# Kernel tuning notes

Measured on AMD Instinct MI355X. Metric: run time of the kernel, lower is better.

## Reference

```python
import jax, jax.numpy as jnp
import numpy as np

NUM_SEQS = 64
NUM_HEADS = 32
NUM_KV_HEADS = 8
HEAD_SIZE = 128
BLOCK_SIZE = 16
X = 8  # key cache vector width (16 bytes / fp16 elem size in vLLM)
NUM_BLOCKS = 4096
MAX_BLOCKS_PER_SEQ = 64
MAX_CTX = MAX_BLOCKS_PER_SEQ * BLOCK_SIZE  # 1024
SCALE = 0.08838834764831845  # 1/sqrt(HEAD_SIZE)
Q_PER_KV = NUM_HEADS // NUM_KV_HEADS


def setup_inputs() -> dict:
    key = jax.random.key(0)
    k0, k1, k2, k3, k4 = jax.random.split(key, 5)
    query = jax.random.normal(k0, (NUM_SEQS, NUM_HEADS, HEAD_SIZE), dtype=jnp.float32)
    key_cache = jax.random.normal(
        k1, (NUM_BLOCKS, NUM_KV_HEADS, HEAD_SIZE // X, BLOCK_SIZE, X), dtype=jnp.float32)
    value_cache = jax.random.normal(
        k2, (NUM_BLOCKS, NUM_KV_HEADS, HEAD_SIZE, BLOCK_SIZE), dtype=jnp.float32)
    block_tables = jax.random.randint(
        k3, (NUM_SEQS, MAX_BLOCKS_PER_SEQ), 0, NUM_BLOCKS, dtype=jnp.int32)
    context_lens = jax.random.randint(k4, (NUM_SEQS,), 1, MAX_CTX + 1, dtype=jnp.int32)
    return {"query": query, "key_cache": key_cache, "value_cache": value_cache,
            "block_tables": block_tables, "context_lens": context_lens}


def _paged_attention(query, key_cache, value_cache, block_tables, context_lens):
    nb = key_cache.shape[0]
    # key cache [nb, kvH, hs//x, bs, x] -> [nb, kvH, bs, hs]
    k_tok = jnp.transpose(key_cache, (0, 1, 3, 2, 4)).reshape(nb, NUM_KV_HEADS, BLOCK_SIZE, HEAD_SIZE)
    # value cache [nb, kvH, hs, bs] -> [nb, kvH, bs, hs]
    v_tok = jnp.transpose(value_cache, (0, 1, 3, 2))
    # gather per-sequence paged KV via block tables: [S, MB, kvH, bs, hs] -> [S, MAX_CTX, kvH, hs]
    keys = k_tok[block_tables].transpose(0, 1, 3, 2, 4).reshape(NUM_SEQS, MAX_CTX, NUM_KV_HEADS, HEAD_SIZE)
    values = v_tok[block_tables].transpose(0, 1, 3, 2, 4).reshape(NUM_SEQS, MAX_CTX, NUM_KV_HEADS, HEAD_SIZE)
    # GQA: group query heads over kv heads. q4: [S, kvH, qpkv, hs]
    q4 = query.reshape(NUM_SEQS, NUM_KV_HEADS, Q_PER_KV, HEAD_SIZE)
    # scores: [S, kvH, qpkv, MAX_CTX]
    scores = jnp.einsum('sgqd,skgd->sgqk', q4, keys) * SCALE
    valid = jnp.arange(MAX_CTX, dtype=jnp.int32)[None, :] < context_lens[:, None]  # [S, K]
    scores = jnp.where(valid[:, None, None, :], scores, jnp.float32(-1e30))
    probs = jax.nn.softmax(scores, axis=-1)
    out = jnp.einsum('sgqk,skgd->sgqd', probs, values)
    return out.reshape(NUM_SEQS, NUM_HEADS, HEAD_SIZE)


def reference(query, key_cache, value_cache, block_tables, context_lens):
    return _paged_attention(query, key_cache, value_cache, block_tables, context_lens)
```

## Files before the change

kernel.cpp:

```cpp
#include <hip/hip_runtime.h>

#define NSEQ   64
#define NHEAD  32
#define KVH    8
#define HS     128
#define BS     16
#define MBPS   64
#define MAXCTX 1024
#define QPKV   4
#define SCALE_F 0.08838834764831845f

__launch_bounds__(256)
__global__ void pa_kernel(const float* __restrict__ q,
                          const float* __restrict__ kc,
                          const float* __restrict__ vc,
                          const int*   __restrict__ bt,
                          const int*   __restrict__ cl,
                          float*       __restrict__ out)
{
    const int seq = blockIdx.x >> 3;
    const int kvh = blockIdx.x & 7;
    const int t   = threadIdx.x;
    const int ctx = cl[seq];
    const int nb  = (ctx + BS - 1) / BS;

    __shared__ __align__(16) float sc[QPKV][MAXCTX + 8];
    __shared__ float qs[QPKV][HS];
    __shared__ float l_inv[QPKV];

    for (int i = t; i < QPKV * HS; i += 256) {
        int g = i >> 7, d = i & 127;
        qs[g][d] = q[((size_t)seq * NHEAD + kvh * QPKV + g) * HS + d];
    }
    __syncthreads();

    const int tok   = t >> 4;
    const int dpart = t & 15;
    float qreg[QPKV][8];
#pragma unroll
    for (int g = 0; g < QPKV; ++g)
#pragma unroll
        for (int j = 0; j < 8; ++j)
            qreg[g][j] = qs[g][dpart * 8 + j];

    const int* btrow = bt + seq * MBPS;
    for (int b = 0; b < nb; ++b) {
        const int blk = btrow[b];
        const float* kptr = kc + ((size_t)blk * KVH + kvh) * (HS * BS)
                               + dpart * (BS * 8) + tok * 8;
        const float4 k0 = *(const float4*)kptr;
        const float4 k1 = *(const float4*)(kptr + 4);
        const float kk[8] = {k0.x,k0.y,k0.z,k0.w,k1.x,k1.y,k1.z,k1.w};
        float p[QPKV];
#pragma unroll
        for (int g = 0; g < QPKV; ++g) {
            float s = 0.f;
#pragma unroll
            for (int j = 0; j < 8; ++j) s += qreg[g][j] * kk[j];
            p[g] = s;
        }
#pragma unroll
        for (int off = 8; off >= 1; off >>= 1)
#pragma unroll
            for (int g = 0; g < QPKV; ++g)
                p[g] += __shfl_xor(p[g], off, 16);
        if (dpart < QPKV)
            sc[dpart][b * BS + tok] = p[dpart] * SCALE_F;
    }
    __syncthreads();

    {
        const int w    = t >> 6;
        const int lane = t & 63;
        float m = -1e30f;
        for (int i = lane; i < ctx; i += 64) m = fmaxf(m, sc[w][i]);
#pragma unroll
        for (int off = 32; off >= 1; off >>= 1) m = fmaxf(m, __shfl_xor(m, off));
        float ssum = 0.f;
        const int lim = nb * BS;
        for (int i = lane; i < lim; i += 64) {
            float v = (i < ctx) ? __expf(sc[w][i] - m) : 0.f;
            sc[w][i] = v;
            ssum += v;
        }
#pragma unroll
        for (int off = 32; off >= 1; off >>= 1) ssum += __shfl_xor(ssum, off);
        if (lane == 0) l_inv[w] = 1.f / ssum;
    }
    __syncthreads();

    const int d  = t >> 1;
    const int th = t & 1;
    float acc[QPKV] = {0.f, 0.f, 0.f, 0.f};
    for (int b = 0; b < nb; ++b) {
        const int blk = btrow[b];
        const float* vptr = vc + ((size_t)blk * KVH + kvh) * (HS * BS)
                               + d * BS + th * 8;
        const float4 v0 = *(const float4*)vptr;
        const float4 v1 = *(const float4*)(vptr + 4);
        const float vv[8] = {v0.x,v0.y,v0.z,v0.w,v1.x,v1.y,v1.z,v1.w};
        const int base = b * BS + th * 8;
#pragma unroll
        for (int g = 0; g < QPKV; ++g) {
            const float4 p0 = *(const float4*)&sc[g][base];
            const float4 p1 = *(const float4*)&sc[g][base + 4];
            acc[g] += p0.x*vv[0] + p0.y*vv[1] + p0.z*vv[2] + p0.w*vv[3]
                    + p1.x*vv[4] + p1.y*vv[5] + p1.z*vv[6] + p1.w*vv[7];
        }
    }
#pragma unroll
    for (int g = 0; g < QPKV; ++g)
        acc[g] += __shfl_xor(acc[g], 1);
    if (th == 0) {
#pragma unroll
        for (int g = 0; g < QPKV; ++g)
            out[((size_t)seq * NHEAD + kvh * QPKV + g) * HS + d] = acc[g] * l_inv[g];
    }
}

extern "C" void kernel_launch(void* const* d_in, const int* in_sizes, int n_in,
                              void* d_out, int out_size, void* d_ws, size_t ws_size,
                              hipStream_t stream) {
    const float* query       = (const float*)d_in[0];
    const float* key_cache   = (const float*)d_in[1];
    const float* value_cache = (const float*)d_in[2];
    const int*   block_tables= (const int*)d_in[3];
    const int*   context_lens= (const int*)d_in[4];
    float* out = (float*)d_out;

    dim3 grid(NSEQ * KVH);
    dim3 block(256);
    pa_kernel<<<grid, block, 0, stream>>>(query, key_cache, value_cache,
                                          block_tables, context_lens, out);
}
```

Measured before the change: 479.7 us.

## Split context into chunks with partial softmax and a separate reduce kernel

Replaces the single per-(sequence, kv-head) kernel with a flash-decoding style split: each workgroup handles an 8-block context chunk, producing a partial output plus its local max and exp-sum in workspace. A second kernel rescales and combines the chunks into the final output. This raises the workgroup count to fill the GPU and reduce load imbalance from variable context lengths, at the cost of an extra launch and workspace traffic. The old kernel is kept as a fallback when workspace is too small.

```diff
diff --git a/kernel.cpp b/kernel.cpp
--- a/kernel.cpp
+++ b/kernel.cpp
@@ -9,6 +9,162 @@
 #define MAXCTX 1024
 #define QPKV   4
 #define SCALE_F 0.08838834764831845f
+
+#define CB     8
+#define CTOK   (CB * BS)
+#define NCHUNK (MBPS / CB)
+#define NPART  (NSEQ * KVH * QPKV * NCHUNK)
+#define WS_BYTES ((size_t)(NPART * HS + 2 * NPART) * 4)
+
+__launch_bounds__(256)
+__global__ void pa_partial(const float* __restrict__ q,
+                           const float* __restrict__ kc,
+                           const float* __restrict__ vc,
+                           const int*   __restrict__ bt,
+                           const int*   __restrict__ cl,
+                           float*       __restrict__ opart,
+                           float*       __restrict__ mpart,
+                           float*       __restrict__ lpart)
+{
+    const int wg  = blockIdx.x;
+    const int kvh = wg & 7;
+    const int c   = (wg >> 3) & (NCHUNK - 1);
+    const int seq = wg >> 6;
+
+    const int ctx = cl[seq];
+    const int nb  = (ctx + BS - 1) >> 4;
+    const int b0  = c * CB;
+    if (b0 >= nb) return;
+    const int nbc = min(nb - b0, CB);
+    const int t   = threadIdx.x;
+
+    __shared__ __align__(16) float sc[QPKV][CTOK + 8];
+    __shared__ float qs[QPKV][HS];
+
+    for (int i = t; i < QPKV * HS; i += 256) {
+        int g = i >> 7, d = i & 127;
+        qs[g][d] = q[((size_t)seq * NHEAD + kvh * QPKV + g) * HS + d];
+    }
+    __syncthreads();
+
+    const int tok   = t >> 4;
+    const int dpart = t & 15;
+    float qreg[QPKV][8];
+#pragma unroll
+    for (int g = 0; g < QPKV; ++g)
+#pragma unroll
+        for (int j = 0; j < 8; ++j)
+            qreg[g][j] = qs[g][dpart * 8 + j];
+
+    const int* btrow = bt + seq * MBPS + b0;
+    for (int b = 0; b < nbc; ++b) {
+        const int blk = btrow[b];
+        const float* kptr = kc + ((size_t)blk * KVH + kvh) * (HS * BS)
+                               + dpart * (BS * 8) + tok * 8;
+        const float4 k0 = *(const float4*)kptr;
+        const float4 k1 = *(const float4*)(kptr + 4);
+        const float kk[8] = {k0.x,k0.y,k0.z,k0.w,k1.x,k1.y,k1.z,k1.w};
+        float p[QPKV];
+#pragma unroll
+        for (int g = 0; g < QPKV; ++g) {
+            float s = 0.f;
+#pragma unroll
+            for (int j = 0; j < 8; ++j) s += qreg[g][j] * kk[j];
+            p[g] = s;
+        }
+#pragma unroll
+        for (int off = 8; off >= 1; off >>= 1)
+#pragma unroll
+            for (int g = 0; g < QPKV; ++g)
+                p[g] += __shfl_xor(p[g], off, 16);
+        if (dpart < QPKV)
+            sc[dpart][b * BS + tok] = p[dpart] * SCALE_F;
+    }
+    __syncthreads();
+
+    {
+        const int w     = t >> 6;
+        const int lane  = t & 63;
+        const int lim   = nbc * BS;
+        const int valid = min(ctx - c * CTOK, lim);
+        float m = -1e30f;
+        for (int i = lane; i < valid; i += 64) m = fmaxf(m, sc[w][i]);
+#pragma unroll
+        for (int off = 32; off >= 1; off >>= 1) m = fmaxf(m, __shfl_xor(m, off));
+        float ssum = 0.f;
+        for (int i = lane; i < lim; i += 64) {
+            float v = (i < valid) ? __expf(sc[w][i] - m) : 0.f;
+            sc[w][i] = v;
+            ssum += v;
+        }
+#pragma unroll
+        for (int off = 32; off >= 1; off >>= 1) ssum += __shfl_xor(ssum, off);
+        if (lane == 0) {
+            const int pidx = ((seq * KVH + kvh) * QPKV + w) * NCHUNK + c;
+            mpart[pidx] = m;
+            lpart[pidx] = ssum;
+        }
+    }
+    __syncthreads();
+
+    const int d  = t >> 1;
+    const int th = t & 1;
+    float acc[QPKV] = {0.f, 0.f, 0.f, 0.f};
+    for (int b = 0; b < nbc; ++b) {
+        const int blk = btrow[b];
+        const float* vptr = vc + ((size_t)blk * KVH + kvh) * (HS * BS)
+                               + d * BS + th * 8;
+        const float4 v0 = *(const float4*)vptr;
+        const float4 v1 = *(const float4*)(vptr + 4);
+        const float vv[8] = {v0.x,v0.y,v0.z,v0.w,v1.x,v1.y,v1.z,v1.w};
+        const int base = b * BS + th * 8;
+#pragma unroll
+        for (int g = 0; g < QPKV; ++g) {
+            const float4 p0 = *(const float4*)&sc[g][base];
+            const float4 p1 = *(const float4*)&sc[g][base + 4];
+            acc[g] += p0.x*vv[0] + p0.y*vv[1] + p0.z*vv[2] + p0.w*vv[3]
+                    + p1.x*vv[4] + p1.y*vv[5] + p1.z*vv[6] + p1.w*vv[7];
+        }
+    }
+#pragma unroll
+    for (int g = 0; g < QPKV; ++g)
+        acc[g] += __shfl_xor(acc[g], 1);
+    if (th == 0) {
+#pragma unroll
+        for (int g = 0; g < QPKV; ++g)
+            opart[((size_t)((seq * KVH + kvh) * QPKV + g) * NCHUNK + c) * HS + d] = acc[g];
+    }
+}
+
+__launch_bounds__(128)
+__global__ void pa_reduce(const float* __restrict__ opart,
+                          const float* __restrict__ mpart,
+                          const float* __restrict__ lpart,
+                          const int*   __restrict__ cl,
+                          float*       __restrict__ out)
+{
+    const int wg  = blockIdx.x;
+    const int seq = wg >> 3;
+    const int d   = threadIdx.x;
+    const int ctx = cl[seq];
+    const int nb  = (ctx + BS - 1) >> 4;
+    const int nch = min((nb + CB - 1) / CB, NCHUNK);
+    const int kvh = wg & 7;
+
+#pragma unroll
+    for (int g = 0; g < QPKV; ++g) {
+        const int base = (wg * QPKV + g) * NCHUNK;
+        float M = -1e30f;
+        for (int c2 = 0; c2 < nch; ++c2) M = fmaxf(M, mpart[base + c2]);
+        float L = 0.f, o = 0.f;
+        for (int c2 = 0; c2 < nch; ++c2) {
+            const float w = __expf(mpart[base + c2] - M);
+            L += lpart[base + c2] * w;
+            o += opart[(size_t)(base + c2) * HS + d] * w;
+        }
+        out[((size_t)seq * NHEAD + kvh * QPKV + g) * HS + d] = o / L;
+    }
+}
 
 __launch_bounds__(256)
 __global__ void pa_kernel(const float* __restrict__ q,
@@ -121,15 +277,24 @@
 extern "C" void kernel_launch(void* const* d_in, const int* in_sizes, int n_in,
                               void* d_out, int out_size, void* d_ws, size_t ws_size,
                               hipStream_t stream) {
-    const float* query       = (const float*)d_in[0];
-    const float* key_cache   = (const float*)d_in[1];
-    const float* value_cache = (const float*)d_in[2];
-    const int*   block_tables= (const int*)d_in[3];
-    const int*   context_lens= (const int*)d_in[4];
+    const float* query        = (const float*)d_in[0];
+    const float* key_cache    = (const float*)d_in[1];
+    const float* value_cache  = (const float*)d_in[2];
+    const int*   block_tables = (const int*)d_in[3];
+    const int*   context_lens = (const int*)d_in[4];
     float* out = (float*)d_out;
 
-    dim3 grid(NSEQ * KVH);
-    dim3 block(256);
-    pa_kernel<<<grid, block, 0, stream>>>(query, key_cache, value_cache,
-                                          block_tables, context_lens, out);
+    if (d_ws != nullptr && ws_size >= WS_BYTES) {
+        float* opart = (float*)d_ws;
+        float* mpart = opart + (size_t)NPART * HS;
+        float* lpart = mpart + NPART;
+        pa_partial<<<dim3(NSEQ * KVH * NCHUNK), dim3(256), 0, stream>>>(
+            query, key_cache, value_cache, block_tables, context_lens,
+            opart, mpart, lpart);
+        pa_reduce<<<dim3(NSEQ * KVH), dim3(128), 0, stream>>>(
+            opart, mpart, lpart, context_lens, out);
+    } else {
+        pa_kernel<<<dim3(NSEQ * KVH), dim3(256), 0, stream>>>(
+            query, key_cache, value_cache, block_tables, context_lens, out);
+    }
 }
```

Result: faster. 467.8 us (-2.5%).
